# Kernel optimization log

Hardware: AMD Instinct MI355X
Metric: run time of the kernel (lower is better)

Reference implementation:

```python
import jax, jax.numpy as jnp
import numpy as np

N, C, L, E, H = 2000, 4, 5000, 64000, 512
REP = 207  # length after conv front-end: floor((floor((5000-11)/4)+1 - 11)/6)+1


def setup_inputs() -> dict:
    key = jax.random.key(0)
    ks = jax.random.split(key, 10)

    def init(k, shape, fan_in):
        return jax.random.normal(k, shape, jnp.float32) / np.sqrt(fan_in).astype(np.float32)

    x = jax.random.normal(ks[0], (N, C, L), jnp.float32)
    edge_index = jax.random.randint(ks[1], (2, E), 0, N)
    return dict(
        x=x, edge_index=edge_index,
        w1=init(ks[2], (16, C, 1), C), b1=jnp.zeros(16, jnp.float32),
        w2=init(ks[3], (4, 4, 11), 4 * 11), b2=jnp.zeros(4, jnp.float32),
        w3=init(ks[4], (1, 4, 11), 4 * 11), b3=jnp.zeros(1, jnp.float32),
        gcn_w=init(ks[5], (REP, H), REP), gcn_b=jnp.zeros(H, jnp.float32),
        lin_w=init(ks[6], (REP, H), REP), lin_b=jnp.zeros(H, jnp.float32),
        gate_w=init(ks[7], (H, H), H), gate_b=jnp.zeros(H, jnp.float32),
        bn_gamma=jnp.ones(H, jnp.float32), bn_beta=jnp.zeros(H, jnp.float32),
    )


def _conv1d(x, w, b, stride):
    # x: [N, Cin, L], w: [Cout, Cin, K] (torch OIH layout), VALID padding
    y = jax.lax.conv_general_dilated(x, w, (stride,), 'VALID',
                                     dimension_numbers=('NCH', 'OIH', 'NCH'))
    return y + b[None, :, None]


def _gcn_conv(feat, edge_index, w, b, n):
    # GCNConv: x@W, add self-loops, sym-normalize, scatter-add, + bias
    h = feat @ w                                      # [N, H]
    loops = jnp.arange(n)
    src = jnp.concatenate([edge_index[0], loops])
    dst = jnp.concatenate([edge_index[1], loops])
    deg = jax.ops.segment_sum(jnp.ones_like(src, h.dtype), dst, num_segments=n)
    dinv = jax.lax.rsqrt(deg)                         # deg >= 1 due to self-loops
    norm = dinv[src] * dinv[dst]                      # [E+N]
    out = jax.ops.segment_sum(h[src] * norm[:, None], dst, num_segments=n)
    return out + b


def reference(x, edge_index, w1, b1, w2, b2, w3, b3,
              gcn_w, gcn_b, lin_w, lin_b, gate_w, gate_b, bn_gamma, bn_beta):
    n = x.shape[0]
    # conv front-end (dropout layers are identity at inference)
    h = jax.nn.relu(_conv1d(x, w1, b1, 1))            # [N, 16, L]
    # MaxPool1d(k=4,s=4) applied on permuted [N, L, 16] == pool over channel dim
    h = h.reshape(n, 4, 4, L).max(axis=2)             # [N, 4, L]
    h = jax.nn.relu(_conv1d(h, w2, b2, 4))            # [N, 4, 1248]
    h = jax.nn.relu(_conv1d(h, w3, b3, 6))            # [N, 1, 207]
    feat = h[:, 0, :]                                 # squeeze -> [N, REP]
    # GCN + gated fusion
    z = jnp.tanh(_gcn_conv(feat, edge_index, gcn_w, gcn_b, n))
    g = jax.nn.sigmoid(z @ gate_w + gate_b)
    xl = feat @ lin_w + lin_b
    out = jax.nn.relu((1.0 - g) * xl + g * z)
    # BatchNorm over node dim (batch statistics, training-mode semantics)
    mean = out.mean(axis=0)
    var = out.var(axis=0)
    out = (out - mean) * jax.lax.rsqrt(var + 1e-5) * bn_gamma + bn_beta
    return out
```

## Files before the change

### kernel.cpp

```cpp
#include <hip/hip_runtime.h>
#include <hip/hip_bf16.h>
#include <cstddef>

#define NN 2000
#define CC 4
#define LL1 5000
#define LL2 1248
#define LL3 207
#define FSTR 208
#define HH 512
#define EE 64000

__device__ float g_feat[NN * FSTR];
__device__ float g_aggf[NN * FSTR];
__device__ float g_z[NN * HH];
__device__ float g_xl[NN * HH];
__device__ float g_obuf[NN * HH];
__device__ float g_dinv[NN];
__device__ float g_colsum[HH];
__device__ float g_colsq[HH];
__device__ int   g_cnt[NN];
__device__ int   g_cursor[NN];
__device__ int   g_off[NN];
__device__ int   g_bucket[EE];

#define MCH 1256
__global__ __launch_bounds__(256) void conv_chain(
    const float* __restrict__ x,
    const float* __restrict__ w1, const float* __restrict__ b1,
    const float* __restrict__ w2, const float* __restrict__ b2,
    const float* __restrict__ w3, const float* __restrict__ b3)
{
    __shared__ __align__(16) float sm[4 * MCH];
    __shared__ __align__(16) float sy[4 * LL2];

    const int tid = threadIdx.x;
    const int node = blockIdx.x;

    if (node < 8) {
        int i = node * 256 + tid;
        if (i < NN) { g_cnt[i] = 0; g_cursor[i] = 0; }
        if (i < HH) { g_colsum[i] = 0.f; g_colsq[i] = 0.f; }
    }

    const float* xb = x + (size_t)node * (CC * LL1);

    float w1r[64], b1r[16];
#pragma unroll
    for (int i = 0; i < 64; ++i) w1r[i] = w1[i];
#pragma unroll
    for (int i = 0; i < 16; ++i) b1r[i] = b1[i];

#pragma unroll 1
    for (int c = 0; c < 4; ++c) {
        const int l0 = 1248 * c;
        for (int g4 = tid; g4 < 314; g4 += 256) {
            const int l = l0 + 4 * g4;
            float xs[4][4];
#pragma unroll
            for (int ch = 0; ch < 4; ++ch)
                *(float4*)xs[ch] = *(const float4*)(xb + ch * LL1 + l);
#pragma unroll
            for (int g = 0; g < 4; ++g) {
                float mv[4];
#pragma unroll
                for (int li = 0; li < 4; ++li) {
                    float best = -1e30f;
#pragma unroll
                    for (int j = 0; j < 4; ++j) {
                        int o = g * 4 + j;
                        float v = b1r[o] + w1r[o*4+0]*xs[0][li] + w1r[o*4+1]*xs[1][li]
                                         + w1r[o*4+2]*xs[2][li] + w1r[o*4+3]*xs[3][li];
                        best = fmaxf(best, v);
                    }
                    mv[li] = fmaxf(best, 0.f);
                }
                *(float4*)&sm[g * MCH + 4 * g4] = make_float4(mv[0], mv[1], mv[2], mv[3]);
            }
        }
        __syncthreads();

        const int T0 = 312 * c;
#pragma unroll 1
        for (int pair = 0; pair < 2; ++pair) {
            const float* wp = w2 + 88 * pair;
            float wo[88];
#pragma unroll
            for (int i = 0; i < 88; ++i) wo[i] = wp[i];
            const float bo0 = b2[2 * pair], bo1 = b2[2 * pair + 1];
            for (int T = tid; T < 312; T += 256) {
                float a0 = bo0, a1 = bo1;
#pragma unroll
                for (int i = 0; i < 4; ++i) {
                    const float* mp = sm + i * MCH + 4 * T;
                    float4 u0 = *(const float4*)mp;
                    float4 u1 = *(const float4*)(mp + 4);
                    float4 u2 = *(const float4*)(mp + 8);
                    float v[12] = {u0.x, u0.y, u0.z, u0.w,
                                   u1.x, u1.y, u1.z, u1.w,
                                   u2.x, u2.y, u2.z, u2.w};
#pragma unroll
                    for (int k = 0; k < 11; ++k) {
                        a0 += wo[i * 11 + k] * v[k];
                        a1 += wo[44 + i * 11 + k] * v[k];
                    }
                }
                sy[(2 * pair) * LL2 + T0 + T]     = fmaxf(a0, 0.f);
                sy[(2 * pair + 1) * LL2 + T0 + T] = fmaxf(a1, 0.f);
            }
        }
        __syncthreads();
    }

    if (tid < FSTR) {
        float acc = 0.f;
        if (tid < LL3) {
            acc = b3[0];
#pragma unroll
            for (int i = 0; i < 4; ++i)
#pragma unroll
                for (int k = 0; k < 11; ++k)
                    acc += w3[i * 11 + k] * sy[i * LL2 + 6 * tid + k];
            acc = fmaxf(acc, 0.f);
        }
        g_feat[(size_t)node * FSTR + tid] = acc;
    }
}

__global__ void edge_count(const int* __restrict__ ei, int E) {
    int e = blockIdx.x * 256 + threadIdx.x;
    if (e < E) atomicAdd(&g_cnt[ei[E + e]], 1);
}

__global__ __launch_bounds__(256) void scan_dinv() {
    __shared__ int a[2048], b[2048];
    int tid = threadIdx.x;
    for (int i = tid; i < 2048; i += 256) a[i] = (i < NN) ? g_cnt[i] : 0;
    __syncthreads();
    int* src = a; int* dst = b;
    for (int d = 1; d < 2048; d <<= 1) {
        for (int i = tid; i < 2048; i += 256)
            dst[i] = src[i] + ((i >= d) ? src[i - d] : 0);
        __syncthreads();
        int* t = src; src = dst; dst = t;
    }
    for (int i = tid; i < NN; i += 256) {
        g_off[i] = src[i] - g_cnt[i];
        g_dinv[i] = rsqrtf(1.0f + (float)g_cnt[i]);
    }
}

__global__ void bucket_fill(const int* __restrict__ ei, int E) {
    int e = blockIdx.x * 256 + threadIdx.x;
    if (e < E) {
        int d = ei[E + e];
        int p = atomicAdd(&g_cursor[d], 1);
        g_bucket[g_off[d] + p] = ei[e];
    }
}

__global__ __launch_bounds__(256) void agg_feat() {
    const int sub = threadIdx.x >> 6;
    const int lane = threadIdx.x & 63;
    const int d = blockIdx.x * 4 + sub;
    if (lane >= 52) return;
    const float di = g_dinv[d];
    const int nb = g_cnt[d];
    const int base = g_off[d];
    const size_t co = (size_t)lane * 4;
    float4 a = *(const float4*)(g_feat + (size_t)d * FSTR + co);
    float ax = a.x * di, ay = a.y * di, az = a.z * di, aw = a.w * di;
    int j = 0;
    for (; j + 1 < nb; j += 2) {
        int s0 = g_bucket[base + j];
        int s1 = g_bucket[base + j + 1];
        float w0 = g_dinv[s0], w1 = g_dinv[s1];
        float4 f0 = *(const float4*)(g_feat + (size_t)s0 * FSTR + co);
        float4 f1 = *(const float4*)(g_feat + (size_t)s1 * FSTR + co);
        ax += f0.x * w0 + f1.x * w1;
        ay += f0.y * w0 + f1.y * w1;
        az += f0.z * w0 + f1.z * w1;
        aw += f0.w * w0 + f1.w * w1;
    }
    if (j < nb) {
        int s = g_bucket[base + j];
        float w = g_dinv[s];
        float4 f = *(const float4*)(g_feat + (size_t)s * FSTR + co);
        ax += f.x * w; ay += f.y * w; az += f.z * w; aw += f.w * w;
    }
    *(float4*)(g_aggf + (size_t)d * FSTR + co) = make_float4(ax * di, ay * di, az * di, aw * di);
}

__global__ __launch_bounds__(256) void gemm_zxl(
    const float* __restrict__ gcn_w, const float* __restrict__ gcn_b,
    const float* __restrict__ lin_w, const float* __restrict__ lin_b)
{
    __shared__ __align__(16) float As[2][16][68];
    __shared__ __align__(16) float Bs[2][16][68];
    const int tid = threadIdx.x;
    const int which = blockIdx.z;
    const float* __restrict__ A = which ? g_feat : g_aggf;
    const float* __restrict__ B = which ? lin_w : gcn_w;
    const float* __restrict__ bias = which ? lin_b : gcn_b;
    float* __restrict__ C = which ? g_xl : g_z;
    const int N0 = blockIdx.x * 64, M0 = blockIdx.y * 64;
    const int ar = tid >> 2, ak = (tid & 3) * 4;
    const int bk = tid >> 4, bn = (tid & 15) * 4;
    const int ty = tid >> 4, tx = tid & 15;
    const int rowA = M0 + ar;

    float acc[16];
#pragma unroll
    for (int i = 0; i < 16; ++i) acc[i] = 0.f;
    const float4 z4 = make_float4(0.f, 0.f, 0.f, 0.f);
    float4 rA, rB;

    rA = (rowA < NN) ? *(const float4*)(A + (size_t)rowA * FSTR + ak) : z4;
    rB = (bk < LL3) ? *(const float4*)(B + (size_t)bk * HH + N0 + bn) : z4;
    As[0][ak+0][ar] = rA.x; As[0][ak+1][ar] = rA.y;
    As[0][ak+2][ar] = rA.z; As[0][ak+3][ar] = rA.w;
    *(float4*)&Bs[0][bk][bn] = rB;
    __syncthreads();

#pragma unroll 1
    for (int kt = 0; kt < 13; ++kt) {
        const int cur = kt & 1;
        if (kt + 1 < 13) {
            const int k0 = (kt + 1) * 16;
            rA = (rowA < NN) ? *(const float4*)(A + (size_t)rowA * FSTR + k0 + ak) : z4;
            const int kb = k0 + bk;
            rB = (kb < LL3) ? *(const float4*)(B + (size_t)kb * HH + N0 + bn) : z4;
        }
#pragma unroll
        for (int k = 0; k < 16; ++k) {
            const float4 a4 = *(const float4*)&As[cur][k][ty * 4];
            const float4 b4 = *(const float4*)&Bs[cur][k][tx * 4];
            const float av[4] = {a4.x, a4.y, a4.z, a4.w};
            const float bv[4] = {b4.x, b4.y, b4.z, b4.w};
#pragma unroll
            for (int i = 0; i < 4; ++i)
#pragma unroll
                for (int j = 0; j < 4; ++j)
                    acc[i * 4 + j] += av[i] * bv[j];
        }
        if (kt + 1 < 13) {
            const int nxt = cur ^ 1;
            As[nxt][ak+0][ar] = rA.x; As[nxt][ak+1][ar] = rA.y;
            As[nxt][ak+2][ar] = rA.z; As[nxt][ak+3][ar] = rA.w;
            *(float4*)&Bs[nxt][bk][bn] = rB;
        }
        __syncthreads();
    }

    const int c0 = N0 + tx * 4;
    const float4 bb = *(const float4*)(bias + c0);
#pragma unroll
    for (int i = 0; i < 4; ++i) {
        const int r = M0 + ty * 4 + i;
        if (r < NN) {
            float4 v = make_float4(acc[i*4+0] + bb.x, acc[i*4+1] + bb.y,
                                   acc[i*4+2] + bb.z, acc[i*4+3] + bb.w);
            if (which == 0) { v.x = tanhf(v.x); v.y = tanhf(v.y); v.z = tanhf(v.z); v.w = tanhf(v.w); }
            *(float4*)(C + (size_t)r * HH + c0) = v;
        }
    }
}

__global__ __launch_bounds__(256) void gemm_gate(
    const float* __restrict__ gate_w, const float* __restrict__ gate_b)
{
    __shared__ __align__(16) float As[2][16][68];
    __shared__ __align__(16) float Bs[2][16][68];
    __shared__ float rs[64], rq[64];
    const int tid = threadIdx.x;
    const float* __restrict__ A = g_z;
    const int N0 = blockIdx.x * 64, M0 = blockIdx.y * 64;
    const int ar = tid >> 2, ak = (tid & 3) * 4;
    const int bk = tid >> 4, bn = (tid & 15) * 4;
    const int ty = tid >> 4, tx = tid & 15;
    const int rowA = M0 + ar;

    float acc[16];
#pragma unroll
    for (int i = 0; i < 16; ++i) acc[i] = 0.f;
    const float4 z4 = make_float4(0.f, 0.f, 0.f, 0.f);
    float4 rA, rB;

    rA = (rowA < NN) ? *(const float4*)(A + (size_t)rowA * HH + ak) : z4;
    rB = *(const float4*)(gate_w + (size_t)bk * HH + N0 + bn);
    As[0][ak+0][ar] = rA.x; As[0][ak+1][ar] = rA.y;
    As[0][ak+2][ar] = rA.z; As[0][ak+3][ar] = rA.w;
    *(float4*)&Bs[0][bk][bn] = rB;
    __syncthreads();

#pragma unroll 1
    for (int kt = 0; kt < 32; ++kt) {
        const int cur = kt & 1;
        if (kt + 1 < 32) {
            const int k0 = (kt + 1) * 16;
            rA = (rowA < NN) ? *(const float4*)(A + (size_t)rowA * HH + k0 + ak) : z4;
            rB = *(const float4*)(gate_w + (size_t)(k0 + bk) * HH + N0 + bn);
        }
#pragma unroll
        for (int k = 0; k < 16; ++k) {
            const float4 a4 = *(const float4*)&As[cur][k][ty * 4];
            const float4 b4 = *(const float4*)&Bs[cur][k][tx * 4];
            const float av[4] = {a4.x, a4.y, a4.z, a4.w};
            const float bv[4] = {b4.x, b4.y, b4.z, b4.w};
#pragma unroll
            for (int i = 0; i < 4; ++i)
#pragma unroll
                for (int j = 0; j < 4; ++j)
                    acc[i * 4 + j] += av[i] * bv[j];
        }
        if (kt + 1 < 32) {
            const int nxt = cur ^ 1;
            As[nxt][ak+0][ar] = rA.x; As[nxt][ak+1][ar] = rA.y;
            As[nxt][ak+2][ar] = rA.z; As[nxt][ak+3][ar] = rA.w;
            *(float4*)&Bs[nxt][bk][bn] = rB;
        }
        __syncthreads();
    }

    const int c0 = N0 + tx * 4;
    const float4 bb = *(const float4*)(gate_b + c0);
    float cs[4] = {0.f, 0.f, 0.f, 0.f}, cq[4] = {0.f, 0.f, 0.f, 0.f};
#pragma unroll
    for (int i = 0; i < 4; ++i) {
        const int r = M0 + ty * 4 + i;
        if (r < NN) {
            const float4 xv = *(const float4*)(g_xl + (size_t)r * HH + c0);
            const float4 zv = *(const float4*)(g_z + (size_t)r * HH + c0);
            const float pre[4] = {acc[i*4+0] + bb.x, acc[i*4+1] + bb.y,
                                  acc[i*4+2] + bb.z, acc[i*4+3] + bb.w};
            const float xa[4] = {xv.x, xv.y, xv.z, xv.w};
            const float za[4] = {zv.x, zv.y, zv.z, zv.w};
            float va[4];
#pragma unroll
            for (int j = 0; j < 4; ++j) {
                float g = 1.f / (1.f + __expf(-pre[j]));
                float v = fmaxf((1.f - g) * xa[j] + g * za[j], 0.f);
                va[j] = v; cs[j] += v; cq[j] += v * v;
            }
            *(float4*)(g_obuf + (size_t)r * HH + c0) = make_float4(va[0], va[1], va[2], va[3]);
        }
    }
    if (tid < 64) { rs[tid] = 0.f; rq[tid] = 0.f; }
    __syncthreads();
#pragma unroll
    for (int j = 0; j < 4; ++j) {
        atomicAdd(&rs[tx * 4 + j], cs[j]);
        atomicAdd(&rq[tx * 4 + j], cq[j]);
    }
    __syncthreads();
    if (tid < 64) {
        atomicAdd(&g_colsum[N0 + tid], rs[tid]);
        atomicAdd(&g_colsq[N0 + tid], rq[tid]);
    }
}

__global__ __launch_bounds__(256) void bn_apply(const float* __restrict__ gamma,
                                                const float* __restrict__ beta,
                                                float* __restrict__ out) {
    int i = blockIdx.x * 256 + threadIdx.x;
    int c = i & (HH - 1);
    float mean = g_colsum[c] * (1.f / (float)NN);
    float var = g_colsq[c] * (1.f / (float)NN) - mean * mean;
    float s = rsqrtf(var + 1e-5f) * gamma[c];
    out[i] = g_obuf[i] * s + (beta[c] - mean * s);
}

extern "C" void kernel_launch(void* const* d_in, const int* in_sizes, int n_in,
                              void* d_out, int out_size, void* d_ws, size_t ws_size,
                              hipStream_t stream) {
    (void)d_ws; (void)ws_size; (void)n_in; (void)out_size;
    const float* x      = (const float*)d_in[0];
    const int*   ei     = (const int*)d_in[1];
    const float* w1     = (const float*)d_in[2];
    const float* b1     = (const float*)d_in[3];
    const float* w2     = (const float*)d_in[4];
    const float* b2     = (const float*)d_in[5];
    const float* w3     = (const float*)d_in[6];
    const float* b3     = (const float*)d_in[7];
    const float* gcn_w  = (const float*)d_in[8];
    const float* gcn_b  = (const float*)d_in[9];
    const float* lin_w  = (const float*)d_in[10];
    const float* lin_b  = (const float*)d_in[11];
    const float* gate_w = (const float*)d_in[12];
    const float* gate_b = (const float*)d_in[13];
    const float* bn_g   = (const float*)d_in[14];
    const float* bn_b   = (const float*)d_in[15];
    float* out = (float*)d_out;
    const int E = in_sizes[1] / 2;

    conv_chain<<<NN, 256, 0, stream>>>(x, w1, b1, w2, b2, w3, b3);
    edge_count<<<(E + 255) / 256, 256, 0, stream>>>(ei, E);
    scan_dinv<<<1, 256, 0, stream>>>();
    bucket_fill<<<(E + 255) / 256, 256, 0, stream>>>(ei, E);
    agg_feat<<<NN / 4, 256, 0, stream>>>();

    gemm_zxl<<<dim3(HH / 64, (NN + 63) / 64, 2), 256, 0, stream>>>(gcn_w, gcn_b, lin_w, lin_b);
    gemm_gate<<<dim3(HH / 64, (NN + 63) / 64), 256, 0, stream>>>(gate_w, gate_b);

    bn_apply<<<(NN * HH) / 256, 256, 0, stream>>>(bn_g, bn_b, out);
}
```

Measured before the change: 367.4 us.

## Prefetch conv input chunks, fuse edge counting, and use a shuffle-based scan

```diff
diff --git a/kernel.cpp b/kernel.cpp
--- a/kernel.cpp
+++ b/kernel.cpp
@@ -26,7 +26,7 @@
 
 #define MCH 1256
 __global__ __launch_bounds__(256) void conv_chain(
-    const float* __restrict__ x,
+    const float* __restrict__ x, const int* __restrict__ ei, const int E,
     const float* __restrict__ w1, const float* __restrict__ b1,
     const float* __restrict__ w2, const float* __restrict__ b2,
     const float* __restrict__ w3, const float* __restrict__ b3)
@@ -37,10 +37,13 @@
     const int tid = threadIdx.x;
     const int node = blockIdx.x;
 
-    if (node < 8) {
+    if (node < 2) {
         int i = node * 256 + tid;
-        if (i < NN) { g_cnt[i] = 0; g_cursor[i] = 0; }
-        if (i < HH) { g_colsum[i] = 0.f; g_colsq[i] = 0.f; }
+        g_colsum[i] = 0.f; g_colsq[i] = 0.f;
+    }
+    if (node < 250) {
+        for (int e = node * 256 + tid; e < E; e += 250 * 256)
+            atomicAdd(&g_cnt[ei[E + e]], 1);
     }
 
     const float* xb = x + (size_t)node * (CC * LL1);
@@ -51,36 +54,53 @@
 #pragma unroll
     for (int i = 0; i < 16; ++i) b1r[i] = b1[i];
 
-#pragma unroll 1
-    for (int c = 0; c < 4; ++c) {
-        const int l0 = 1248 * c;
-        for (int g4 = tid; g4 < 314; g4 += 256) {
-            const int l = l0 + 4 * g4;
-            float xs[4][4];
-#pragma unroll
-            for (int ch = 0; ch < 4; ++ch)
-                *(float4*)xs[ch] = *(const float4*)(xb + ch * LL1 + l);
-#pragma unroll
-            for (int g = 0; g < 4; ++g) {
-                float mv[4];
-#pragma unroll
-                for (int li = 0; li < 4; ++li) {
-                    float best = -1e30f;
-#pragma unroll
-                    for (int j = 0; j < 4; ++j) {
-                        int o = g * 4 + j;
-                        float v = b1r[o] + w1r[o*4+0]*xs[0][li] + w1r[o*4+1]*xs[1][li]
-                                         + w1r[o*4+2]*xs[2][li] + w1r[o*4+3]*xs[3][li];
-                        best = fmaxf(best, v);
+    float4 xA[2][4], xB[2][4];
+
+    auto issueL = [&](int cc, float4 (&dst)[2][4]) {
+#pragma unroll
+        for (int it = 0; it < 2; ++it) {
+            const int g4 = tid + it * 256;
+            if (g4 < 314) {
+                const int l = 1248 * cc + 4 * g4;
+#pragma unroll
+                for (int ch = 0; ch < 4; ++ch)
+                    dst[it][ch] = *(const float4*)(xb + ch * LL1 + l);
+            }
+        }
+    };
+
+    auto stage1 = [&](float4 (&src)[2][4]) {
+#pragma unroll
+        for (int it = 0; it < 2; ++it) {
+            const int g4 = tid + it * 256;
+            if (g4 < 314) {
+                float xs[4][4];
+#pragma unroll
+                for (int ch = 0; ch < 4; ++ch)
+                    *(float4*)xs[ch] = src[it][ch];
+#pragma unroll
+                for (int g = 0; g < 4; ++g) {
+                    float mv[4];
+#pragma unroll
+                    for (int li = 0; li < 4; ++li) {
+                        float best = -1e30f;
+#pragma unroll
+                        for (int j = 0; j < 4; ++j) {
+                            int o = g * 4 + j;
+                            float v = b1r[o] + w1r[o*4+0]*xs[0][li] + w1r[o*4+1]*xs[1][li]
+                                             + w1r[o*4+2]*xs[2][li] + w1r[o*4+3]*xs[3][li];
+                            best = fmaxf(best, v);
+                        }
+                        mv[li] = fmaxf(best, 0.f);
                     }
-                    mv[li] = fmaxf(best, 0.f);
+                    *(float4*)&sm[g * MCH + 4 * g4] = make_float4(mv[0], mv[1], mv[2], mv[3]);
                 }
-                *(float4*)&sm[g * MCH + 4 * g4] = make_float4(mv[0], mv[1], mv[2], mv[3]);
             }
         }
-        __syncthreads();
-
-        const int T0 = 312 * c;
+    };
+
+    auto stage2 = [&](int cc) {
+        const int T0 = 312 * cc;
 #pragma unroll 1
         for (int pair = 0; pair < 2; ++pair) {
             const float* wp = w2 + 88 * pair;
@@ -109,8 +129,16 @@
                 sy[(2 * pair + 1) * LL2 + T0 + T] = fmaxf(a1, 0.f);
             }
         }
-        __syncthreads();
-    }
+    };
+
+    issueL(0, xA);
+    issueL(1, xB);
+    stage1(xA); __syncthreads(); stage2(0); __syncthreads();
+    issueL(2, xA);
+    stage1(xB); __syncthreads(); stage2(1); __syncthreads();
+    issueL(3, xB);
+    stage1(xA); __syncthreads(); stage2(2); __syncthreads();
+    stage1(xB); __syncthreads(); stage2(3); __syncthreads();
 
     if (tid < FSTR) {
         float acc = 0.f;
@@ -127,26 +155,37 @@
     }
 }
 
-__global__ void edge_count(const int* __restrict__ ei, int E) {
-    int e = blockIdx.x * 256 + threadIdx.x;
-    if (e < E) atomicAdd(&g_cnt[ei[E + e]], 1);
-}
-
 __global__ __launch_bounds__(256) void scan_dinv() {
-    __shared__ int a[2048], b[2048];
-    int tid = threadIdx.x;
-    for (int i = tid; i < 2048; i += 256) a[i] = (i < NN) ? g_cnt[i] : 0;
+    const int tid = threadIdx.x;
+    const int base = tid * 8;
+    int c[8];
+#pragma unroll
+    for (int k = 0; k < 8; ++k) c[k] = (base + k < NN) ? g_cnt[base + k] : 0;
+    int pre[8]; int s = 0;
+#pragma unroll
+    for (int k = 0; k < 8; ++k) { pre[k] = s; s += c[k]; }
+    const int lane = tid & 63;
+    int ws = s;
+#pragma unroll
+    for (int d = 1; d < 64; d <<= 1) {
+        int t = __shfl_up(ws, d, 64);
+        if (lane >= d) ws += t;
+    }
+    __shared__ int wsum[4];
+    const int wid = tid >> 6;
+    if (lane == 63) wsum[wid] = ws;
     __syncthreads();
-    int* src = a; int* dst = b;
-    for (int d = 1; d < 2048; d <<= 1) {
-        for (int i = tid; i < 2048; i += 256)
-            dst[i] = src[i] + ((i >= d) ? src[i - d] : 0);
-        __syncthreads();
-        int* t = src; src = dst; dst = t;
-    }
-    for (int i = tid; i < NN; i += 256) {
-        g_off[i] = src[i] - g_cnt[i];
-        g_dinv[i] = rsqrtf(1.0f + (float)g_cnt[i]);
+    int woff = 0;
+#pragma unroll
+    for (int w = 0; w < 4; ++w) if (w < wid) woff += wsum[w];
+    const int toff = woff + ws - s;
+#pragma unroll
+    for (int k = 0; k < 8; ++k) {
+        const int i = base + k;
+        if (i < NN) {
+            g_off[i] = toff + pre[k];
+            g_dinv[i] = rsqrtf(1.0f + (float)c[k]);
+        }
     }
 }
 
@@ -362,6 +401,10 @@
 __global__ __launch_bounds__(256) void bn_apply(const float* __restrict__ gamma,
                                                 const float* __restrict__ beta,
                                                 float* __restrict__ out) {
+    if (blockIdx.x < 8) {
+        int i = blockIdx.x * 256 + threadIdx.x;
+        if (i < NN) { g_cnt[i] = 0; g_cursor[i] = 0; }
+    }
     int i = blockIdx.x * 256 + threadIdx.x;
     int c = i & (HH - 1);
     float mean = g_colsum[c] * (1.f / (float)NN);
@@ -393,8 +436,7 @@
     float* out = (float*)d_out;
     const int E = in_sizes[1] / 2;
 
-    conv_chain<<<NN, 256, 0, stream>>>(x, w1, b1, w2, b2, w3, b3);
-    edge_count<<<(E + 255) / 256, 256, 0, stream>>>(ei, E);
+    conv_chain<<<NN, 256, 0, stream>>>(x, ei, E, w1, b1, w2, b2, w3, b3);
     scan_dinv<<<1, 256, 0, stream>>>();
     bucket_fill<<<(E + 255) / 256, 256, 0, stream>>>(ei, E);
     agg_feat<<<NN / 4, 256, 0, stream>>>();
```

Result: no change. 369.3 us (+0.5%).
